# Kernel optimization log

Measured on AMD Instinct MI355X. Metric: run time of the kernel, lower is better.

Reference implementation:

```python
import jax, jax.numpy as jnp
import numpy as np

GROUPS = 32
EPS = 1e-5

def setup_inputs() -> dict:
    key = jax.random.key(0)
    ks = jax.random.split(key, 10)
    B, H, W, C = 2, 64, 64, 512
    s = 1.0 / np.sqrt(C)
    return {
        "x": jax.random.normal(ks[0], (B, H, W, C), dtype=jnp.float32),
        "gamma": jnp.ones((C,), jnp.float32),
        "beta": jnp.zeros((C,), jnp.float32),
        "wq": jax.random.normal(ks[1], (C, C), jnp.float32) * s,
        "bq": jnp.zeros((C,), jnp.float32),
        "wk": jax.random.normal(ks[2], (C, C), jnp.float32) * s,
        "bk": jnp.zeros((C,), jnp.float32),
        "wv": jax.random.normal(ks[3], (C, C), jnp.float32) * s,
        "bv": jnp.zeros((C,), jnp.float32),
        "wp": jax.random.normal(ks[4], (C, C), jnp.float32) * s,
        "bp": jnp.zeros((C,), jnp.float32),
    }

def _group_norm(x, gamma, beta):
    B, H, W, C = x.shape
    xg = x.reshape(B, H, W, GROUPS, C // GROUPS)
    mean = jnp.mean(xg, axis=(1, 2, 4), keepdims=True)
    var = jnp.var(xg, axis=(1, 2, 4), keepdims=True)
    xg = (xg - mean) * jax.lax.rsqrt(var + EPS)
    return xg.reshape(B, H, W, C) * gamma + beta

def reference(x, gamma, beta, wq, bq, wk, bk, wv, bv, wp, bp):
    B, H, W, C = x.shape
    h_ = _group_norm(x, gamma, beta)
    # 1x1 convs are per-pixel linear maps
    q = jnp.einsum("bhwc,cd->bhwd", h_, wq) + bq
    k = jnp.einsum("bhwc,cd->bhwd", h_, wk) + bk
    v = jnp.einsum("bhwc,cd->bhwd", h_, wv) + bv
    q = q.reshape(B, H * W, C)
    k = k.reshape(B, H * W, C)
    v = v.reshape(B, H * W, C)
    scale = C ** (-0.5)
    attn = jax.nn.softmax(jnp.einsum("bqc,bkc->bqk", q, k) * scale, axis=-1)
    out = jnp.einsum("bqk,bkc->bqc", attn, v).reshape(B, H, W, C)
    proj = jnp.einsum("bhwc,cd->bhwd", out, wp) + bp
    return x + proj
```

## Files before the change

kernel.cpp:

```cpp
#include <hip/hip_runtime.h>
#include <hip/hip_bf16.h>
#include <cstdint>
#include <cstddef>

typedef __bf16 bf16;
typedef bf16 bf16x8 __attribute__((ext_vector_type(8)));
typedef bf16 bf16x4 __attribute__((ext_vector_type(4)));
typedef float floatx4 __attribute__((ext_vector_type(4)));
typedef int intx8 __attribute__((ext_vector_type(8)));
typedef int intx4 __attribute__((ext_vector_type(4)));

#define DEVI __device__ __forceinline__

#define C_  512
#define HW_ 4096
#define B_  2
#define M_  8192
#define TK  64


DEVI floatx4 mfma16(bf16x8 a, bf16x8 b, floatx4 c) {
  return __builtin_amdgcn_mfma_f32_16x16x32_bf16(a, b, c, 0, 0, 0);
}

DEVI floatx4 mfma_fp8(intx8 a, intx8 b, floatx4 c) {
  return __builtin_amdgcn_mfma_scale_f32_16x16x128_f8f6f4(a, b, c, 0, 0,
                                                          0, 127, 0, 127);
}

DEVI void gload16(const void* g, void* lds) {
  using gp = const __attribute__((address_space(1))) unsigned int*;
  using lp = __attribute__((address_space(3))) unsigned int*;
  __builtin_amdgcn_global_load_lds(
      reinterpret_cast<gp>(reinterpret_cast<uintptr_t>(g)),
      reinterpret_cast<lp>((unsigned int)(uintptr_t)lds), 16, 0, 0);
}

template <int N> DEVI void wait_vmcnt() {
  if constexpr (N == 0)       asm volatile("s_waitcnt vmcnt(0)" ::: "memory");
  else if constexpr (N == 6)  asm volatile("s_waitcnt vmcnt(6)" ::: "memory");
  else if constexpr (N == 8)  asm volatile("s_waitcnt vmcnt(8)" ::: "memory");
  else if constexpr (N == 12) asm volatile("s_waitcnt vmcnt(12)" ::: "memory");
  else if constexpr (N == 16) asm volatile("s_waitcnt vmcnt(16)" ::: "memory");
  else static_assert(N == 0, "unsupported vmcnt literal");
}

DEVI uint32_t f32_to_fp8(float x) {
  return (uint32_t)__builtin_amdgcn_cvt_pk_fp8_f32(x, x, 0, false) & 0xffu;
}
DEVI int pack4_fp8(float a, float b, float c, float d) {
  int pk = __builtin_amdgcn_cvt_pk_fp8_f32(a, b, 0, false);
  return __builtin_amdgcn_cvt_pk_fp8_f32(c, d, pk, true);
}

__global__ __launch_bounds__(256) void gn_part(const float* __restrict__ x,
                                               float* __restrict__ pp,
                                               float* __restrict__ l) {
  int blk = blockIdx.x;
  int t = threadIdx.x;
  if (t < 16) l[blk * 16 + t] = 0.f;
  int batch = blk >> 8;
  int pix0 = (blk & 255) * 16;
  int c4 = (t & 127) << 2;
  int ph = t >> 7;
  const float* px = x + (size_t)batch * HW_ * C_ + (size_t)(pix0 + ph) * C_ + c4;
  float s1 = 0.f, s2 = 0.f;
#pragma unroll
  for (int i = 0; i < 8; i++) {
    float4 v = *reinterpret_cast<const float4*>(px + (size_t)i * 2 * C_);
    s1 += v.x + v.y + v.z + v.w;
    s2 += v.x * v.x + v.y * v.y + v.z * v.z + v.w * v.w;
  }
  __shared__ float l1[256], l2[256];
  l1[t] = s1; l2[t] = s2;
  __syncthreads();
  if (t < 32) {
    float a = 0.f, b2 = 0.f;
#pragma unroll
    for (int j = 0; j < 4; j++) {
      a  += l1[t * 4 + j] + l1[t * 4 + j + 128];
      b2 += l2[t * 4 + j] + l2[t * 4 + j + 128];
    }
    pp[blk * 32 + t] = a;
    pp[512 * 32 + blk * 32 + t] = b2;
  }
}

__global__ __launch_bounds__(256) void finish_wtrans(
    const float* __restrict__ pp, float* __restrict__ stats,
    const float* __restrict__ wq, const float* __restrict__ wk,
    const float* __restrict__ wv, const float* __restrict__ wp,
    uint8_t* __restrict__ w8, bf16* __restrict__ wtp) {
  int t = threadIdx.x;
  if (blockIdx.x < 64) {
    int bg = blockIdx.x;
    int b = bg >> 5, g = bg & 31;
    float s1 = pp[(b * 256 + t) * 32 + g];
    float s2 = pp[512 * 32 + (b * 256 + t) * 32 + g];
    for (int off = 32; off; off >>= 1) {
      s1 += __shfl_down(s1, off);
      s2 += __shfl_down(s2, off);
    }
    __shared__ float r1[4], r2[4];
    int wid = t >> 6;
    if ((t & 63) == 0) { r1[wid] = s1; r2[wid] = s2; }
    __syncthreads();
    if (t == 0) {
      s1 = r1[0] + r1[1] + r1[2] + r1[3];
      s2 = r2[0] + r2[1] + r2[2] + r2[3];
      float inv = 1.0f / (HW_ * 16);
      float mean = s1 * inv;
      float var  = s2 * inv - mean * mean;
      stats[bg]      = mean;
      stats[64 + bg] = rsqrtf(var + 1e-5f);
    }
    return;
  }
  int id = blockIdx.x - 64;
  int z = id >> 8;
  int k0 = ((id >> 4) & 15) * 32, n0 = (id & 15) * 32;
  const float* w = (z == 0) ? wq : (z == 1) ? wk : (z == 2) ? wv : wp;
  __shared__ float tt[32][33];
  int r = t >> 5, cc = t & 31;
  for (int i = 0; i < 4; i++) {
    int rr = r + i * 8;
    tt[rr][cc] = w[(size_t)(k0 + rr) * C_ + n0 + cc];
  }
  __syncthreads();
  if (z < 3) {
    uint8_t* dst = w8 + (size_t)z * C_ * C_;
    for (int i = 0; i < 4; i++) {
      int rr = r + i * 8;
      dst[(size_t)(n0 + rr) * C_ + k0 + cc] = (uint8_t)f32_to_fp8(tt[cc][rr]);
    }
  } else {
    for (int i = 0; i < 4; i++) {
      int rr = r + i * 8;
      wtp[(size_t)(n0 + rr) * C_ + k0 + cc] = (bf16)tt[cc][rr];
    }
  }
}

__global__ __launch_bounds__(256) void gn_apply(const float* __restrict__ x,
                                                const float* __restrict__ gamma,
                                                const float* __restrict__ beta,
                                                const float* __restrict__ stats,
                                                uint8_t* __restrict__ h8) {
  int idx = blockIdx.x * 256 + threadIdx.x;
  int m  = idx >> 7;
  int c4 = (idx & 127) << 2;
  int b = m >> 12;
  int g = c4 >> 4;
  float mean = stats[(b << 5) + g];
  float rs   = stats[64 + (b << 5) + g];
  const float4 xv = *reinterpret_cast<const float4*>(x + (size_t)m * C_ + c4);
  const float4 gv = *reinterpret_cast<const float4*>(gamma + c4);
  const float4 bv = *reinterpret_cast<const float4*>(beta + c4);
  int pk = pack4_fp8((xv.x - mean) * rs * gv.x + bv.x,
                     (xv.y - mean) * rs * gv.y + bv.y,
                     (xv.z - mean) * rs * gv.z + bv.z,
                     (xv.w - mean) * rs * gv.w + bv.w);
  *reinterpret_cast<int*>(h8 + (size_t)m * C_ + c4) = pk;
}

template <int BM, int BN, int MT, int NT>
DEVI void gemm_main(const bf16* __restrict__ A, int lda,
                    const bf16* __restrict__ Bt, int ldb,
                    int K, floatx4 (&acc)[MT][NT]) {
  constexpr int WCOLS = BN / (NT * 16);
  constexpr int NLD = BM / 32 + BN / 32;
  static_assert(NLD == 6 || NLD == 8, "vmcnt literals support 6/8");
  __shared__ __align__(16) bf16 As[3][BM * TK];
  __shared__ __align__(16) bf16 Bs[3][BN * TK];
  int tid = threadIdx.x;
  int w = tid >> 6, lane = tid & 63;
  int wrow = w / WCOLS, wcol = w % WCOLS;
  int col = lane & 15, quad = lane >> 4;
#pragma unroll
  for (int mt = 0; mt < MT; mt++)
#pragma unroll
    for (int nt = 0; nt < NT; nt++)
      acc[mt][nt] = floatx4{0.f, 0.f, 0.f, 0.f};

  auto stage = [&](int k0, bf16* as, bf16* bs) {
#pragma unroll
    for (int i = 0; i < BM / 32; i++) {
      int id = tid + i * 256;
      int r = id >> 3, wd = id & 7;
      gload16(A + (size_t)r * lda + k0 + ((wd ^ (r & 7)) << 3), as + id * 8);
    }
#pragma unroll
    for (int i = 0; i < BN / 32; i++) {
      int id = tid + i * 256;
      int r = id >> 3, wd = id & 7;
      gload16(Bt + (size_t)r * ldb + k0 + ((wd ^ (r & 7)) << 3), bs + id * 8);
    }
  };
  auto compute = [&](const bf16* sa, const bf16* sb) {
#pragma unroll
    for (int kk = 0; kk < 2; kk++) {
      bf16x8 af[MT], bfr[NT];
#pragma unroll
      for (int mt = 0; mt < MT; mt++) {
        int rA = wrow * MT * 16 + mt * 16 + col;
        af[mt] = *reinterpret_cast<const bf16x8*>(
            sa + rA * TK + (((kk * 4 + quad) ^ (rA & 7)) << 3));
      }
#pragma unroll
      for (int nt = 0; nt < NT; nt++) {
        int rB = wcol * NT * 16 + nt * 16 + col;
        bfr[nt] = *reinterpret_cast<const bf16x8*>(
            sb + rB * TK + (((kk * 4 + quad) ^ (rB & 7)) << 3));
      }
#pragma unroll
      for (int mt = 0; mt < MT; mt++)
#pragma unroll
        for (int nt = 0; nt < NT; nt++)
          acc[mt][nt] = mfma16(af[mt], bfr[nt], acc[mt][nt]);
    }
  };

  bf16 *a0 = &As[0][0], *a1 = &As[1][0], *a2 = &As[2][0];
  bf16 *b0 = &Bs[0][0], *b1 = &Bs[1][0], *b2 = &Bs[2][0];
  int nIter = K / TK;
  stage(0, a0, b0);
  stage(TK, a1, b1);
  for (int t = 0; t < nIter; t++) {
    if (t + 2 < nIter) {
      stage((t + 2) * TK, a2, b2);
      wait_vmcnt<2 * NLD>();
    } else if (t + 1 < nIter) {
      wait_vmcnt<NLD>();
    } else {
      wait_vmcnt<0>();
    }
    asm volatile("s_barrier" ::: "memory");
    compute(a0, b0);
    if (t + 1 < nIter) {
      asm volatile("s_waitcnt lgkmcnt(0)" ::: "memory");
      asm volatile("s_barrier" ::: "memory");
    }
    bf16* tp;
    tp = a0; a0 = a1; a1 = a2; a2 = tp;
    tp = b0; b0 = b1; b1 = b2; b2 = tp;
  }
}

template <int BM, int BN, int MT, int NT>
DEVI void gemm_fp8(const uint8_t* __restrict__ A, int lda,
                   const uint8_t* __restrict__ Bt, int ldb,
                   int K, floatx4 (&acc)[MT][NT]) {
  constexpr int WCOLS = BN / (NT * 16);
  constexpr int NLD = BM / 32 + BN / 32;
  static_assert(NLD == 6 || NLD == 8, "vmcnt literals support 6/8");
  __shared__ __align__(16) uint8_t As[3][BM * 128];
  __shared__ __align__(16) uint8_t Bs[3][BN * 128];
  int tid = threadIdx.x;
  int w = tid >> 6, lane = tid & 63;
  int wrow = w / WCOLS, wcol = w % WCOLS;
  int col = lane & 15, quad = lane >> 4;
#pragma unroll
  for (int mt = 0; mt < MT; mt++)
#pragma unroll
    for (int nt = 0; nt < NT; nt++)
      acc[mt][nt] = floatx4{0.f, 0.f, 0.f, 0.f};

  auto stage = [&](int k0, uint8_t* as, uint8_t* bs) {
#pragma unroll
    for (int i = 0; i < BM / 32; i++) {
      int id = tid + i * 256;
      int r = id >> 3, wd = id & 7;
      gload16(A + (size_t)r * lda + k0 + ((wd ^ (r & 7)) << 4), as + id * 16);
    }
#pragma unroll
    for (int i = 0; i < BN / 32; i++) {
      int id = tid + i * 256;
      int r = id >> 3, wd = id & 7;
      gload16(Bt + (size_t)r * ldb + k0 + ((wd ^ (r & 7)) << 4), bs + id * 16);
    }
  };
  auto compute = [&](const uint8_t* sa, const uint8_t* sb) {
    intx8 af[MT], bfr[NT];
#pragma unroll
    for (int mt = 0; mt < MT; mt++) {
      int rA = wrow * MT * 16 + mt * 16 + col;
      const uint8_t* rowp = sa + (size_t)rA * 128;
      intx4 lo = *reinterpret_cast<const intx4*>(
          rowp + (((2 * quad) ^ (rA & 7)) << 4));
      intx4 hi = *reinterpret_cast<const intx4*>(
          rowp + (((2 * quad + 1) ^ (rA & 7)) << 4));
      af[mt] = __builtin_shufflevector(lo, hi, 0, 1, 2, 3, 4, 5, 6, 7);
    }
#pragma unroll
    for (int nt = 0; nt < NT; nt++) {
      int rB = wcol * NT * 16 + nt * 16 + col;
      const uint8_t* rowp = sb + (size_t)rB * 128;
      intx4 lo = *reinterpret_cast<const intx4*>(
          rowp + (((2 * quad) ^ (rB & 7)) << 4));
      intx4 hi = *reinterpret_cast<const intx4*>(
          rowp + (((2 * quad + 1) ^ (rB & 7)) << 4));
      bfr[nt] = __builtin_shufflevector(lo, hi, 0, 1, 2, 3, 4, 5, 6, 7);
    }
#pragma unroll
    for (int mt = 0; mt < MT; mt++)
#pragma unroll
      for (int nt = 0; nt < NT; nt++)
        acc[mt][nt] = mfma_fp8(af[mt], bfr[nt], acc[mt][nt]);
  };

  uint8_t *a0 = &As[0][0], *a1 = &As[1][0], *a2 = &As[2][0];
  uint8_t *b0 = &Bs[0][0], *b1 = &Bs[1][0], *b2 = &Bs[2][0];
  int nIter = K >> 7;
  stage(0, a0, b0);
  stage(128, a1, b1);
  for (int t = 0; t < nIter; t++) {
    if (t + 2 < nIter) {
      stage((t + 2) << 7, a2, b2);
      wait_vmcnt<2 * NLD>();
    } else if (t + 1 < nIter) {
      wait_vmcnt<NLD>();
    } else {
      wait_vmcnt<0>();
    }
    asm volatile("s_barrier" ::: "memory");
    compute(a0, b0);
    if (t + 1 < nIter) {
      asm volatile("s_waitcnt lgkmcnt(0)" ::: "memory");
      asm volatile("s_barrier" ::: "memory");
    }
    uint8_t* tp;
    tp = a0; a0 = a1; a1 = a2; a2 = tp;
    tp = b0; b0 = b1; b1 = b2; b2 = tp;
  }
}

__global__ __launch_bounds__(256) void gemm_qkv(const uint8_t* __restrict__ h8,
                                                const uint8_t* __restrict__ w8,
                                                const float* __restrict__ bq,
                                                const float* __restrict__ bk,
                                                const float* __restrict__ bv,
                                                uint8_t* __restrict__ q8,
                                                uint8_t* __restrict__ k8,
                                                uint8_t* __restrict__ vt8) {
  int z = blockIdx.z;
  int m0 = blockIdx.y * 128, n0 = blockIdx.x * 64;
  floatx4 acc[2][4];
  gemm_fp8<128, 64, 2, 4>(h8 + (size_t)m0 * C_, C_,
                          w8 + (size_t)z * C_ * C_ + (size_t)n0 * C_, C_, C_, acc);
  int tid = threadIdx.x, w = tid >> 6, lane = tid & 63;
  int col = lane & 15, quad = lane >> 4;
  const float* bias = (z == 0) ? bq : (z == 1) ? bk : bv;
  if (z < 2) {
    uint8_t* out = (z == 0) ? q8 : k8;
#pragma unroll
    for (int mt = 0; mt < 2; mt++)
#pragma unroll
      for (int nt = 0; nt < 4; nt++) {
        int n = n0 + nt * 16 + col;
        float bb = bias[n];
#pragma unroll
        for (int r = 0; r < 4; r++) {
          int m = m0 + w * 32 + mt * 16 + quad * 4 + r;
          out[(size_t)m * C_ + n] = (uint8_t)f32_to_fp8(acc[mt][nt][r] + bb);
        }
      }
  } else {
#pragma unroll
    for (int mt = 0; mt < 2; mt++)
#pragma unroll
      for (int nt = 0; nt < 4; nt++) {
        int n = n0 + nt * 16 + col;
        float bb = bias[n];
        int mbase = m0 + w * 32 + mt * 16 + quad * 4;
        int b = mbase >> 12;
        int s = mbase & 4095;
        int pk = pack4_fp8(acc[mt][nt][0] + bb, acc[mt][nt][1] + bb,
                           acc[mt][nt][2] + bb, acc[mt][nt][3] + bb);
        *reinterpret_cast<int*>(vt8 + ((size_t)b * C_ + n) * HW_ + s) = pk;
      }
  }
}

__global__ __launch_bounds__(256) void gemm_qk(const uint8_t* __restrict__ q8,
                                               const uint8_t* __restrict__ k8,
                                               uint8_t* __restrict__ P8,
                                               float* __restrict__ l) {
  int b = blockIdx.z;
  int fid = blockIdx.y * 32 + blockIdx.x;
  int nid = (fid & 7) * 256 + (fid >> 3);
  int m0 = (nid & 31) * 128, n0 = (nid >> 5) * 64;
  floatx4 acc[2][4];
  gemm_fp8<128, 64, 2, 4>(q8 + ((size_t)b * HW_ + m0) * C_, C_,
                          k8 + ((size_t)b * HW_ + n0) * C_, C_, C_, acc);
  int tid = threadIdx.x, w = tid >> 6, lane = tid & 63;
  int col = lane & 15, quad = lane >> 4;
  const float sl2e = 0.044194173824159216f * 1.4426950408889634f;
  uint8_t* Pb = P8 + (size_t)b * HW_ * HW_;
  float* lb = l + (size_t)b * HW_;
#pragma unroll
  for (int mt = 0; mt < 2; mt++) {
    float rs[4] = {0.f, 0.f, 0.f, 0.f};
#pragma unroll
    for (int nt = 0; nt < 4; nt++) {
      int n = n0 + nt * 16 + col;
      float p0 = exp2f(acc[mt][nt][0] * sl2e);
      float p1 = exp2f(acc[mt][nt][1] * sl2e);
      float p2 = exp2f(acc[mt][nt][2] * sl2e);
      float p3 = exp2f(acc[mt][nt][3] * sl2e);
      int pk = pack4_fp8(p0, p1, p2, p3);
      size_t base = (size_t)(m0 + w * 32 + mt * 16 + quad * 4) * HW_ + n;
      Pb[base]           = (uint8_t)pk;
      Pb[base + HW_]     = (uint8_t)((unsigned)pk >> 8);
      Pb[base + 2 * HW_] = (uint8_t)((unsigned)pk >> 16);
      Pb[base + 3 * HW_] = (uint8_t)((unsigned)pk >> 24);
      rs[0] += p0; rs[1] += p1; rs[2] += p2; rs[3] += p3;
    }
#pragma unroll
    for (int off = 1; off < 16; off <<= 1)
#pragma unroll
      for (int r = 0; r < 4; r++)
        rs[r] += __shfl_xor(rs[r], off);
    if (col == 0)
#pragma unroll
      for (int r = 0; r < 4; r++)
        atomicAdd(&lb[m0 + w * 32 + mt * 16 + quad * 4 + r], rs[r]);
  }
}

__global__ __launch_bounds__(256) void gemm_pv(const uint8_t* __restrict__ P8,
                                               const uint8_t* __restrict__ vt8,
                                               const float* __restrict__ l,
                                               bf16* __restrict__ o) {
  int b = blockIdx.z;
  int fid = blockIdx.y * 32 + blockIdx.x;
  int xcd = fid & 7, i = fid >> 3;
  int m0 = (xcd * 4 + (i & 3)) * 128;
  int n0 = (i >> 2) * 64;
  floatx4 acc[2][4];
  gemm_fp8<128, 64, 2, 4>(P8 + (size_t)b * HW_ * HW_ + (size_t)m0 * HW_, HW_,
                          vt8 + ((size_t)b * C_ + n0) * HW_, HW_, HW_, acc);
  int tid = threadIdx.x, w = tid >> 6, lane = tid & 63;
  int col = lane & 15, quad = lane >> 4;
  const float* lb = l + (size_t)b * HW_;
  bf16* ob = o + (size_t)b * HW_ * C_;
#pragma unroll
  for (int mt = 0; mt < 2; mt++)
#pragma unroll
    for (int r = 0; r < 4; r++) {
      int m = m0 + w * 32 + mt * 16 + quad * 4 + r;
      float inv = 1.0f / lb[m];
#pragma unroll
      for (int nt = 0; nt < 4; nt++) {
        int n = n0 + nt * 16 + col;
        ob[(size_t)m * C_ + n] = (bf16)(acc[mt][nt][r] * inv);
      }
    }
}

__global__ __launch_bounds__(256) void gemm_proj(const bf16* __restrict__ o,
                                                 const bf16* __restrict__ wtp,
                                                 const float* __restrict__ bp,
                                                 const float* __restrict__ x,
                                                 float* __restrict__ out) {
  int m0 = blockIdx.y * 128, n0 = blockIdx.x * 64;
  floatx4 acc[2][4];
  gemm_main<128, 64, 2, 4>(o + (size_t)m0 * C_, C_, wtp + (size_t)n0 * C_, C_, C_, acc);
  int tid = threadIdx.x, w = tid >> 6, lane = tid & 63;
  int col = lane & 15, quad = lane >> 4;
#pragma unroll
  for (int mt = 0; mt < 2; mt++)
#pragma unroll
    for (int nt = 0; nt < 4; nt++) {
      int n = n0 + nt * 16 + col;
      float bb = bp[n];
#pragma unroll
      for (int r = 0; r < 4; r++) {
        int m = m0 + w * 32 + mt * 16 + quad * 4 + r;
        out[(size_t)m * C_ + n] = x[(size_t)m * C_ + n] + acc[mt][nt][r] + bb;
      }
    }
}

extern "C" void kernel_launch(void* const* d_in, const int* in_sizes, int n_in,
                              void* d_out, int out_size, void* d_ws, size_t ws_size,
                              hipStream_t stream) {
  const float* x     = (const float*)d_in[0];
  const float* gamma = (const float*)d_in[1];
  const float* beta  = (const float*)d_in[2];
  const float* wq    = (const float*)d_in[3];
  const float* bq    = (const float*)d_in[4];
  const float* wk    = (const float*)d_in[5];
  const float* bk    = (const float*)d_in[6];
  const float* wv    = (const float*)d_in[7];
  const float* bv    = (const float*)d_in[8];
  const float* wp    = (const float*)d_in[9];
  const float* bp    = (const float*)d_in[10];
  float* out = (float*)d_out;

  char* w8s = (char*)d_ws;
  float* stats = (float*)(w8s);
  float* l     = (float*)(w8s + 65536u);
  float* pp    = (float*)(w8s + 393216u);
  uint8_t* w8  = (uint8_t*)(w8s + (1u << 20));
  bf16* wtp    = (bf16*)(w8s + (2u << 20));
  uint8_t* h8  = (uint8_t*)(w8s + (4u << 20));
  bf16* o      = (bf16*)(w8s + (8u << 20));
  uint8_t* q8  = (uint8_t*)(w8s + (16u << 20));
  uint8_t* k8  = (uint8_t*)(w8s + (20u << 20));
  uint8_t* vt8 = (uint8_t*)(w8s + (24u << 20));
  uint8_t* P8  = (uint8_t*)(w8s + (28u << 20));

  gn_part<<<512, 256, 0, stream>>>(x, pp, l);
  finish_wtrans<<<1088, 256, 0, stream>>>(pp, stats, wq, wk, wv, wp, w8, wtp);
  gn_apply<<<4096, 256, 0, stream>>>(x, gamma, beta, stats, h8);
  gemm_qkv<<<dim3(C_ / 64, M_ / 128, 3), 256, 0, stream>>>(h8, w8, bq, bk, bv, q8, k8, vt8);
  gemm_qk<<<dim3(HW_ / 128, HW_ / 64, B_), 256, 0, stream>>>(q8, k8, P8, l);
  gemm_pv<<<dim3(HW_ / 128, C_ / 64, B_), 256, 0, stream>>>(P8, vt8, l, o);
  gemm_proj<<<dim3(C_ / 64, M_ / 128, 1), 256, 0, stream>>>(o, wtp, bp, x, out);
}
```

Before: 193.2 us.

## Use 128x128 double-buffered FP8 tiles for QKV and QK GEMMs

Adds a double-buffered FP8 GEMM path with 128x128 block tiles (4x4 MFMA tiles per wave, 2x2 wave grid) and switches the QKV projection and QK^T score kernels to it, with grids and epilogue indexing adjusted to match. The larger tile halves the number of blocks and raises data reuse per loaded byte. The cost is more accumulator registers and less pipelining depth (two LDS stages instead of three). The PV and output projection kernels keep the triple-buffered 128x64 path, now specialised with hard-coded vmcnt values.

```diff
diff --git a/kernel.cpp b/kernel.cpp
--- a/kernel.cpp
+++ b/kernel.cpp
@@ -41,7 +41,6 @@
   else if constexpr (N == 6)  asm volatile("s_waitcnt vmcnt(6)" ::: "memory");
   else if constexpr (N == 8)  asm volatile("s_waitcnt vmcnt(8)" ::: "memory");
   else if constexpr (N == 12) asm volatile("s_waitcnt vmcnt(12)" ::: "memory");
-  else if constexpr (N == 16) asm volatile("s_waitcnt vmcnt(16)" ::: "memory");
   else static_assert(N == 0, "unsupported vmcnt literal");
 }
 
@@ -164,12 +163,12 @@
 }
 
 template <int BM, int BN, int MT, int NT>
-DEVI void gemm_main(const bf16* __restrict__ A, int lda,
-                    const bf16* __restrict__ Bt, int ldb,
-                    int K, floatx4 (&acc)[MT][NT]) {
+DEVI void gemm_main_tb(const bf16* __restrict__ A, int lda,
+                       const bf16* __restrict__ Bt, int ldb,
+                       int K, floatx4 (&acc)[MT][NT]) {
   constexpr int WCOLS = BN / (NT * 16);
   constexpr int NLD = BM / 32 + BN / 32;
-  static_assert(NLD == 6 || NLD == 8, "vmcnt literals support 6/8");
+  static_assert(NLD == 6, "3-buf path sized for 128x64");
   __shared__ __align__(16) bf16 As[3][BM * TK];
   __shared__ __align__(16) bf16 Bs[3][BN * TK];
   int tid = threadIdx.x;
@@ -228,9 +227,9 @@
   for (int t = 0; t < nIter; t++) {
     if (t + 2 < nIter) {
       stage((t + 2) * TK, a2, b2);
-      wait_vmcnt<2 * NLD>();
+      wait_vmcnt<12>();
     } else if (t + 1 < nIter) {
-      wait_vmcnt<NLD>();
+      wait_vmcnt<6>();
     } else {
       wait_vmcnt<0>();
     }
@@ -247,14 +246,14 @@
 }
 
 template <int BM, int BN, int MT, int NT>
-DEVI void gemm_fp8(const uint8_t* __restrict__ A, int lda,
-                   const uint8_t* __restrict__ Bt, int ldb,
-                   int K, floatx4 (&acc)[MT][NT]) {
+DEVI void gemm_fp8_db(const uint8_t* __restrict__ A, int lda,
+                      const uint8_t* __restrict__ Bt, int ldb,
+                      int K, floatx4 (&acc)[MT][NT]) {
   constexpr int WCOLS = BN / (NT * 16);
   constexpr int NLD = BM / 32 + BN / 32;
-  static_assert(NLD == 6 || NLD == 8, "vmcnt literals support 6/8");
-  __shared__ __align__(16) uint8_t As[3][BM * 128];
-  __shared__ __align__(16) uint8_t Bs[3][BN * 128];
+  static_assert(NLD == 8, "dbuf path sized for 128x128");
+  __shared__ __align__(16) uint8_t As[2][BM * 128];
+  __shared__ __align__(16) uint8_t Bs[2][BN * 128];
   int tid = threadIdx.x;
   int w = tid >> 6, lane = tid & 63;
   int wrow = w / WCOLS, wcol = w % WCOLS;
@@ -308,6 +307,88 @@
         acc[mt][nt] = mfma_fp8(af[mt], bfr[nt], acc[mt][nt]);
   };
 
+  uint8_t *s0a = &As[0][0], *s0b = &Bs[0][0];
+  uint8_t *s1a = &As[1][0], *s1b = &Bs[1][0];
+  stage(0, s0a, s0b);
+  int nIter = K >> 7;
+  for (int t = 0; t < nIter - 1; t++) {
+    stage((t + 1) << 7, s1a, s1b);
+    wait_vmcnt<8>();
+    asm volatile("s_barrier" ::: "memory");
+    compute(s0a, s0b);
+    asm volatile("s_waitcnt lgkmcnt(0)" ::: "memory");
+    asm volatile("s_barrier" ::: "memory");
+    uint8_t* tp;
+    tp = s0a; s0a = s1a; s1a = tp;
+    tp = s0b; s0b = s1b; s1b = tp;
+  }
+  wait_vmcnt<0>();
+  asm volatile("s_barrier" ::: "memory");
+  compute(s0a, s0b);
+}
+
+template <int BM, int BN, int MT, int NT>
+DEVI void gemm_fp8_tb(const uint8_t* __restrict__ A, int lda,
+                      const uint8_t* __restrict__ Bt, int ldb,
+                      int K, floatx4 (&acc)[MT][NT]) {
+  constexpr int WCOLS = BN / (NT * 16);
+  constexpr int NLD = BM / 32 + BN / 32;
+  static_assert(NLD == 6, "3-buf path sized for 128x64");
+  __shared__ __align__(16) uint8_t As[3][BM * 128];
+  __shared__ __align__(16) uint8_t Bs[3][BN * 128];
+  int tid = threadIdx.x;
+  int w = tid >> 6, lane = tid & 63;
+  int wrow = w / WCOLS, wcol = w % WCOLS;
+  int col = lane & 15, quad = lane >> 4;
+#pragma unroll
+  for (int mt = 0; mt < MT; mt++)
+#pragma unroll
+    for (int nt = 0; nt < NT; nt++)
+      acc[mt][nt] = floatx4{0.f, 0.f, 0.f, 0.f};
+
+  auto stage = [&](int k0, uint8_t* as, uint8_t* bs) {
+#pragma unroll
+    for (int i = 0; i < BM / 32; i++) {
+      int id = tid + i * 256;
+      int r = id >> 3, wd = id & 7;
+      gload16(A + (size_t)r * lda + k0 + ((wd ^ (r & 7)) << 4), as + id * 16);
+    }
+#pragma unroll
+    for (int i = 0; i < BN / 32; i++) {
+      int id = tid + i * 256;
+      int r = id >> 3, wd = id & 7;
+      gload16(Bt + (size_t)r * ldb + k0 + ((wd ^ (r & 7)) << 4), bs + id * 16);
+    }
+  };
+  auto compute = [&](const uint8_t* sa, const uint8_t* sb) {
+    intx8 af[MT], bfr[NT];
+#pragma unroll
+    for (int mt = 0; mt < MT; mt++) {
+      int rA = wrow * MT * 16 + mt * 16 + col;
+      const uint8_t* rowp = sa + (size_t)rA * 128;
+      intx4 lo = *reinterpret_cast<const intx4*>(
+          rowp + (((2 * quad) ^ (rA & 7)) << 4));
+      intx4 hi = *reinterpret_cast<const intx4*>(
+          rowp + (((2 * quad + 1) ^ (rA & 7)) << 4));
+      af[mt] = __builtin_shufflevector(lo, hi, 0, 1, 2, 3, 4, 5, 6, 7);
+    }
+#pragma unroll
+    for (int nt = 0; nt < NT; nt++) {
+      int rB = wcol * NT * 16 + nt * 16 + col;
+      const uint8_t* rowp = sb + (size_t)rB * 128;
+      intx4 lo = *reinterpret_cast<const intx4*>(
+          rowp + (((2 * quad) ^ (rB & 7)) << 4));
+      intx4 hi = *reinterpret_cast<const intx4*>(
+          rowp + (((2 * quad + 1) ^ (rB & 7)) << 4));
+      bfr[nt] = __builtin_shufflevector(lo, hi, 0, 1, 2, 3, 4, 5, 6, 7);
+    }
+#pragma unroll
+    for (int mt = 0; mt < MT; mt++)
+#pragma unroll
+      for (int nt = 0; nt < NT; nt++)
+        acc[mt][nt] = mfma_fp8(af[mt], bfr[nt], acc[mt][nt]);
+  };
+
   uint8_t *a0 = &As[0][0], *a1 = &As[1][0], *a2 = &As[2][0];
   uint8_t *b0 = &Bs[0][0], *b1 = &Bs[1][0], *b2 = &Bs[2][0];
   int nIter = K >> 7;
@@ -316,9 +397,9 @@
   for (int t = 0; t < nIter; t++) {
     if (t + 2 < nIter) {
       stage((t + 2) << 7, a2, b2);
-      wait_vmcnt<2 * NLD>();
+      wait_vmcnt<12>();
     } else if (t + 1 < nIter) {
-      wait_vmcnt<NLD>();
+      wait_vmcnt<6>();
     } else {
       wait_vmcnt<0>();
     }
@@ -343,35 +424,36 @@
                                                 uint8_t* __restrict__ k8,
                                                 uint8_t* __restrict__ vt8) {
   int z = blockIdx.z;
-  int m0 = blockIdx.y * 128, n0 = blockIdx.x * 64;
-  floatx4 acc[2][4];
-  gemm_fp8<128, 64, 2, 4>(h8 + (size_t)m0 * C_, C_,
-                          w8 + (size_t)z * C_ * C_ + (size_t)n0 * C_, C_, C_, acc);
+  int m0 = blockIdx.x * 128, n0 = blockIdx.y * 128;
+  floatx4 acc[4][4];
+  gemm_fp8_db<128, 128, 4, 4>(h8 + (size_t)m0 * C_, C_,
+                              w8 + (size_t)z * C_ * C_ + (size_t)n0 * C_, C_, C_, acc);
   int tid = threadIdx.x, w = tid >> 6, lane = tid & 63;
+  int wrow = w >> 1, wcol = w & 1;
   int col = lane & 15, quad = lane >> 4;
   const float* bias = (z == 0) ? bq : (z == 1) ? bk : bv;
   if (z < 2) {
     uint8_t* out = (z == 0) ? q8 : k8;
 #pragma unroll
-    for (int mt = 0; mt < 2; mt++)
+    for (int mt = 0; mt < 4; mt++)
 #pragma unroll
       for (int nt = 0; nt < 4; nt++) {
-        int n = n0 + nt * 16 + col;
+        int n = n0 + wcol * 64 + nt * 16 + col;
         float bb = bias[n];
 #pragma unroll
         for (int r = 0; r < 4; r++) {
-          int m = m0 + w * 32 + mt * 16 + quad * 4 + r;
+          int m = m0 + wrow * 64 + mt * 16 + quad * 4 + r;
           out[(size_t)m * C_ + n] = (uint8_t)f32_to_fp8(acc[mt][nt][r] + bb);
         }
       }
   } else {
 #pragma unroll
-    for (int mt = 0; mt < 2; mt++)
+    for (int mt = 0; mt < 4; mt++)
 #pragma unroll
       for (int nt = 0; nt < 4; nt++) {
-        int n = n0 + nt * 16 + col;
+        int n = n0 + wcol * 64 + nt * 16 + col;
         float bb = bias[n];
-        int mbase = m0 + w * 32 + mt * 16 + quad * 4;
+        int mbase = m0 + wrow * 64 + mt * 16 + quad * 4;
         int b = mbase >> 12;
         int s = mbase & 4095;
         int pk = pack4_fp8(acc[mt][nt][0] + bb, acc[mt][nt][1] + bb,
@@ -387,28 +469,29 @@
                                                float* __restrict__ l) {
   int b = blockIdx.z;
   int fid = blockIdx.y * 32 + blockIdx.x;
-  int nid = (fid & 7) * 256 + (fid >> 3);
-  int m0 = (nid & 31) * 128, n0 = (nid >> 5) * 64;
-  floatx4 acc[2][4];
-  gemm_fp8<128, 64, 2, 4>(q8 + ((size_t)b * HW_ + m0) * C_, C_,
-                          k8 + ((size_t)b * HW_ + n0) * C_, C_, C_, acc);
+  int nid = (fid & 7) * 128 + (fid >> 3);
+  int m0 = (nid & 31) * 128, n0 = (nid >> 5) * 128;
+  floatx4 acc[4][4];
+  gemm_fp8_db<128, 128, 4, 4>(q8 + ((size_t)b * HW_ + m0) * C_, C_,
+                              k8 + ((size_t)b * HW_ + n0) * C_, C_, C_, acc);
   int tid = threadIdx.x, w = tid >> 6, lane = tid & 63;
+  int wrow = w >> 1, wcol = w & 1;
   int col = lane & 15, quad = lane >> 4;
   const float sl2e = 0.044194173824159216f * 1.4426950408889634f;
   uint8_t* Pb = P8 + (size_t)b * HW_ * HW_;
   float* lb = l + (size_t)b * HW_;
 #pragma unroll
-  for (int mt = 0; mt < 2; mt++) {
+  for (int mt = 0; mt < 4; mt++) {
     float rs[4] = {0.f, 0.f, 0.f, 0.f};
 #pragma unroll
     for (int nt = 0; nt < 4; nt++) {
-      int n = n0 + nt * 16 + col;
+      int n = n0 + wcol * 64 + nt * 16 + col;
       float p0 = exp2f(acc[mt][nt][0] * sl2e);
       float p1 = exp2f(acc[mt][nt][1] * sl2e);
       float p2 = exp2f(acc[mt][nt][2] * sl2e);
       float p3 = exp2f(acc[mt][nt][3] * sl2e);
       int pk = pack4_fp8(p0, p1, p2, p3);
-      size_t base = (size_t)(m0 + w * 32 + mt * 16 + quad * 4) * HW_ + n;
+      size_t base = (size_t)(m0 + wrow * 64 + mt * 16 + quad * 4) * HW_ + n;
       Pb[base]           = (uint8_t)pk;
       Pb[base + HW_]     = (uint8_t)((unsigned)pk >> 8);
       Pb[base + 2 * HW_] = (uint8_t)((unsigned)pk >> 16);
@@ -423,7 +506,7 @@
     if (col == 0)
 #pragma unroll
       for (int r = 0; r < 4; r++)
-        atomicAdd(&lb[m0 + w * 32 + mt * 16 + quad * 4 + r], rs[r]);
+        atomicAdd(&lb[m0 + wrow * 64 + mt * 16 + quad * 4 + r], rs[r]);
   }
 }
 
@@ -437,8 +520,8 @@
   int m0 = (xcd * 4 + (i & 3)) * 128;
   int n0 = (i >> 2) * 64;
   floatx4 acc[2][4];
-  gemm_fp8<128, 64, 2, 4>(P8 + (size_t)b * HW_ * HW_ + (size_t)m0 * HW_, HW_,
-                          vt8 + ((size_t)b * C_ + n0) * HW_, HW_, HW_, acc);
+  gemm_fp8_tb<128, 64, 2, 4>(P8 + (size_t)b * HW_ * HW_ + (size_t)m0 * HW_, HW_,
+                             vt8 + ((size_t)b * C_ + n0) * HW_, HW_, HW_, acc);
   int tid = threadIdx.x, w = tid >> 6, lane = tid & 63;
   int col = lane & 15, quad = lane >> 4;
   const float* lb = l + (size_t)b * HW_;
@@ -464,7 +547,7 @@
                                                  float* __restrict__ out) {
   int m0 = blockIdx.y * 128, n0 = blockIdx.x * 64;
   floatx4 acc[2][4];
-  gemm_main<128, 64, 2, 4>(o + (size_t)m0 * C_, C_, wtp + (size_t)n0 * C_, C_, C_, acc);
+  gemm_main_tb<128, 64, 2, 4>(o + (size_t)m0 * C_, C_, wtp + (size_t)n0 * C_, C_, C_, acc);
   int tid = threadIdx.x, w = tid >> 6, lane = tid & 63;
   int col = lane & 15, quad = lane >> 4;
 #pragma unroll
@@ -513,8 +596,8 @@
   gn_part<<<512, 256, 0, stream>>>(x, pp, l);
   finish_wtrans<<<1088, 256, 0, stream>>>(pp, stats, wq, wk, wv, wp, w8, wtp);
   gn_apply<<<4096, 256, 0, stream>>>(x, gamma, beta, stats, h8);
-  gemm_qkv<<<dim3(C_ / 64, M_ / 128, 3), 256, 0, stream>>>(h8, w8, bq, bk, bv, q8, k8, vt8);
-  gemm_qk<<<dim3(HW_ / 128, HW_ / 64, B_), 256, 0, stream>>>(q8, k8, P8, l);
+  gemm_qkv<<<dim3(M_ / 128, C_ / 128, 3), 256, 0, stream>>>(h8, w8, bq, bk, bv, q8, k8, vt8);
+  gemm_qk<<<dim3(HW_ / 128, HW_ / 128, B_), 256, 0, stream>>>(q8, k8, P8, l);
   gemm_pv<<<dim3(HW_ / 128, C_ / 64, B_), 256, 0, stream>>>(P8, vt8, l, o);
   gemm_proj<<<dim3(C_ / 64, M_ / 128, 1), 256, 0, stream>>>(o, wtp, bp, x, out);
 }
```

Result: faster. 179.0 us (-7.4%).
